# Kernel optimization log

Hardware: AMD Instinct MI355X
Metric: run time of the kernel (lower is better)

## Reference

```python
import jax, jax.numpy as jnp
import numpy as np

B, L, D, H, FFN = 4, 1024, 1024, 16, 4096
DPH = D // H
EPS = 1e-5

def layer_norm(x, g, b):
    mu = jnp.mean(x, axis=-1, keepdims=True)
    var = jnp.mean(jnp.square(x - mu), axis=-1, keepdims=True)
    return (x - mu) * jax.lax.rsqrt(var + EPS) * g + b

def setup_inputs() -> dict:
    key = jax.random.key(0)
    ks = jax.random.split(key, 12)
    s = 0.02
    return {
        "inputs": jax.random.normal(ks[0], (B, L, D), dtype=jnp.float32),
        "Wq": jax.random.normal(ks[1], (D, D), dtype=jnp.float32) * s,
        "bq": jnp.zeros((D,), jnp.float32),
        "Wk": jax.random.normal(ks[2], (D, D), dtype=jnp.float32) * s,
        "bk": jnp.zeros((D,), jnp.float32),
        "Wv": jax.random.normal(ks[3], (D, D), dtype=jnp.float32) * s,
        "bv": jnp.zeros((D,), jnp.float32),
        "Wo": jax.random.normal(ks[4], (D, D), dtype=jnp.float32) * s,
        "bo": jnp.zeros((D,), jnp.float32),
        "ln1_g": jnp.ones((D,), jnp.float32),
        "ln1_b": jnp.zeros((D,), jnp.float32),
        "W1": jax.random.normal(ks[5], (D, FFN), dtype=jnp.float32) * s,  # conv1d k=1 == linear
        "b1": jnp.zeros((FFN,), jnp.float32),
        "W2": jax.random.normal(ks[6], (FFN, D), dtype=jnp.float32) * s,
        "b2": jnp.zeros((D,), jnp.float32),
        "ln2_g": jnp.ones((D,), jnp.float32),
        "ln2_b": jnp.zeros((D,), jnp.float32),
    }

def reference(inputs, Wq, bq, Wk, bk, Wv, bv, Wo, bo, ln1_g, ln1_b,
              W1, b1, W2, b2, ln2_g, ln2_b):
    residual = inputs
    # QKV projections, then the original's raw view(B*H, L, DPH) split (NOT a transpose split)
    q = (inputs @ Wq + bq).reshape(B * H, L, DPH)
    k = (inputs @ Wk + bk).reshape(B * H, L, DPH)
    v = (inputs @ Wv + bv).reshape(B * H, L, DPH)
    scale = DPH ** -0.5
    scores = jnp.einsum('bqd,bkd->bqk', q, k) * scale  # [B*H, L, L]
    attention = jax.nn.softmax(scores, axis=-1)
    context = jnp.einsum('bqk,bkd->bqd', attention, v).reshape(B, L, D)
    out = context @ Wo + bo
    out = layer_norm(residual + out, ln1_g, ln1_b)
    # Positionwise FFN: two 1x1 conv1d == two linears with relu
    ffn = jax.nn.relu(out @ W1 + b1) @ W2 + b2
    out = layer_norm(out + ffn, ln2_g, ln2_b)
    return out, attention
```

## Files before the change

### kernel.cpp

```cpp
#include <hip/hip_runtime.h>
#include <hip/hip_bf16.h>
#include <stdint.h>


using bf16_t  = __hip_bfloat16;
using short8  = __attribute__((ext_vector_type(8))) short;
using short4v = __attribute__((ext_vector_type(4))) short;
using f32x4   = __attribute__((ext_vector_type(4))) float;

#define DEV static __device__ __forceinline__

DEV short bfbits(float f) {
  bf16_t h = __float2bfloat16(f);
  union { bf16_t h; short s; } u; u.h = h; return u.s;
}

DEV void gload_lds16(const bf16_t* g, bf16_t* lds) {
  __builtin_amdgcn_global_load_lds(
      (const __attribute__((address_space(1))) void*)g,
      (__attribute__((address_space(3))) void*)lds, 16, 0, 0);
}

__global__ __launch_bounds__(256) void k_f32_to_bf16(const float* __restrict__ in,
                                                     bf16_t* __restrict__ out) {
  size_t i = ((size_t)blockIdx.x * 256 + threadIdx.x) * 4;
  f32x4 x = *(const f32x4*)(in + i);
  short4v o;
  o[0] = bfbits(x[0]); o[1] = bfbits(x[1]); o[2] = bfbits(x[2]); o[3] = bfbits(x[3]);
  *(short4v*)((short*)out + i) = o;
}

__global__ __launch_bounds__(256) void k_transpose_f32_bf16(const float* __restrict__ in,
                                                            bf16_t* __restrict__ out,
                                                            int R, int C) {
  __shared__ float tile[32][33];
  int tx = threadIdx.x & 31, ty = threadIdx.x >> 5;
  int r0 = blockIdx.y * 32, c0 = blockIdx.x * 32;
  #pragma unroll
  for (int i = 0; i < 4; ++i)
    tile[ty + i * 8][tx] = in[(size_t)(r0 + ty + i * 8) * C + c0 + tx];
  __syncthreads();
  #pragma unroll
  for (int i = 0; i < 4; ++i)
    out[(size_t)(c0 + ty + i * 8) * R + r0 + tx] = __float2bfloat16(tile[tx][ty + i * 8]);
}

__global__ __launch_bounds__(256) void k_transpose4_f32_bf16(
    const float* __restrict__ w0, const float* __restrict__ w1,
    const float* __restrict__ w2, const float* __restrict__ w3,
    bf16_t* __restrict__ o0, bf16_t* __restrict__ o1,
    bf16_t* __restrict__ o2, bf16_t* __restrict__ o3) {
  __shared__ float tile[32][33];
  const int zz = blockIdx.z;
  const float* in = zz == 0 ? w0 : zz == 1 ? w1 : zz == 2 ? w2 : w3;
  bf16_t* out = zz == 0 ? o0 : zz == 1 ? o1 : zz == 2 ? o2 : o3;
  int tx = threadIdx.x & 31, ty = threadIdx.x >> 5;
  int r0 = blockIdx.y * 32, c0 = blockIdx.x * 32;
  #pragma unroll
  for (int i = 0; i < 4; ++i)
    tile[ty + i * 8][tx] = in[(size_t)(r0 + ty + i * 8) * 1024 + c0 + tx];
  __syncthreads();
  #pragma unroll
  for (int i = 0; i < 4; ++i)
    out[(size_t)(c0 + ty + i * 8) * 1024 + r0 + tx] = __float2bfloat16(tile[tx][ty + i * 8]);
}

__global__ __launch_bounds__(256) void k_transpose_bf16_b(const bf16_t* __restrict__ in,
                                                          bf16_t* __restrict__ out,
                                                          int R, int C, long sIn, long sOut) {
  __shared__ bf16_t tile[32][33];
  const bf16_t* inz = in + (size_t)blockIdx.z * sIn;
  bf16_t* outz = out + (size_t)blockIdx.z * sOut;
  int tx = threadIdx.x & 31, ty = threadIdx.x >> 5;
  int r0 = blockIdx.y * 32, c0 = blockIdx.x * 32;
  #pragma unroll
  for (int i = 0; i < 4; ++i)
    tile[ty + i * 8][tx] = inz[(size_t)(r0 + ty + i * 8) * C + c0 + tx];
  __syncthreads();
  #pragma unroll
  for (int i = 0; i < 4; ++i)
    outz[(size_t)(c0 + ty + i * 8) * R + r0 + tx] = tile[tx][ty + i * 8];
}

template<int BM, int BN, bool ALPHA, bool BIAS, bool RELU, bool RESID,
         bool OUTF, bool OUTB, bool QKV3>
__global__ __launch_bounds__(256)
void k_gemm_bt(const bf16_t* __restrict__ A, const bf16_t* __restrict__ Bt,
               float* __restrict__ Cf, bf16_t* __restrict__ Cb,
               const float* __restrict__ bias, const float* __restrict__ bias2,
               const float* __restrict__ bias3, const float* __restrict__ resid,
               int Kdim, int lda, int ldb, int ldc, float alpha) {
  constexpr int BK = 32;
  constexpr int WTM = BM / 2, WTN = BN / 2;
  constexpr int MI = WTM / 16, NI = WTN / 16;
  __shared__ __align__(16) bf16_t sA[BM * BK];
  __shared__ __align__(16) bf16_t sB[BN * BK];

  const int tid = threadIdx.x;
  const int lane = tid & 63;
  const int wv = tid >> 6;
  const int wm = wv & 1, wn = wv >> 1;

  const int gx = gridDim.x;
  const int total = gx * gridDim.y;
  const int lin = blockIdx.y * gx + blockIdx.x;
  const int swz = (lin & 7) * (total >> 3) + (lin >> 3);
  const size_t m0 = (size_t)(swz / gx) * BM;
  const size_t n0 = (size_t)(swz % gx) * BN;

  f32x4 acc[MI][NI] = {};

  const int rr = lane >> 2, cc = (lane & 3) * 8;
  const bf16_t* Arow = A + (m0 + rr) * (size_t)lda + cc;
  const bf16_t* Brow = Bt + (n0 + rr) * (size_t)ldb + cc;

  const int fm = wm * WTM + (lane & 15);
  const int fn = wn * WTN + (lane & 15);
  const int fk = (lane >> 4) * 8;

  for (int k0 = 0; k0 < Kdim; k0 += BK) {
    #pragma unroll
    for (int j = 0; j < BM / 64; ++j) {
      int c = j * 4 + wv;
      gload_lds16(Arow + (size_t)c * 16 * lda + k0, sA + c * 512);
    }
    #pragma unroll
    for (int j = 0; j < BN / 64; ++j) {
      int c = j * 4 + wv;
      gload_lds16(Brow + (size_t)c * 16 * ldb + k0, sB + c * 512);
    }
    __syncthreads();

    short8 av[MI], bvv[NI];
    #pragma unroll
    for (int mi = 0; mi < MI; ++mi) av[mi] = *(const short8*)(sA + (fm + mi * 16) * BK + fk);
    #pragma unroll
    for (int ni = 0; ni < NI; ++ni) bvv[ni] = *(const short8*)(sB + (fn + ni * 16) * BK + fk);
    #pragma unroll
    for (int mi = 0; mi < MI; ++mi)
      #pragma unroll
      for (int ni = 0; ni < NI; ++ni)
        acc[mi][ni] = __builtin_amdgcn_mfma_f32_16x16x32_bf16(av[mi], bvv[ni],
                                                              acc[mi][ni], 0, 0, 0);
    __syncthreads();
  }

  const int tz = QKV3 ? (int)(n0 >> 10) : 0;
  const float* bp = BIAS ? (QKV3 ? (tz == 0 ? bias : (tz == 1 ? bias2 : bias3))
                                 : bias) : nullptr;
  bf16_t* cb = QKV3 ? (Cb + (size_t)tz * 4194304) : Cb;
  const float qscale = (QKV3 && tz == 0) ? 0.125f : 1.0f;
  const int col0 = (int)n0 + wn * WTN + (lane & 15);
  const int row0 = (int)m0 + wm * WTM + ((lane >> 4) << 2);
  #pragma unroll
  for (int ni = 0; ni < NI; ++ni) {
    const int col = col0 + ni * 16;
    const int colw = QKV3 ? (col & 1023) : col;
    const float bval = BIAS ? bp[colw] : 0.0f;
    #pragma unroll
    for (int mi = 0; mi < MI; ++mi) {
      #pragma unroll
      for (int r = 0; r < 4; ++r) {
        int row = row0 + mi * 16 + r;
        float v = acc[mi][ni][r];
        if (ALPHA) v *= alpha;
        v += bval;
        if (QKV3) v *= qscale;
        size_t off = (size_t)row * ldc + colw;
        if (RESID) v += resid[off];
        if (RELU) v = fmaxf(v, 0.0f);
        if (OUTF) Cf[off] = v;
        if (OUTB) cb[off] = __float2bfloat16(v);
      }
    }
  }
}

__global__ __launch_bounds__(256) void k_flash_attn(const bf16_t* __restrict__ Qb,
                                                    const bf16_t* __restrict__ Kb,
                                                    const bf16_t* __restrict__ Vt,
                                                    float* __restrict__ attn,
                                                    bf16_t* __restrict__ ctx) {
  __shared__ __align__(16) bf16_t sK[2][64][64];
  __shared__ __align__(16) bf16_t sV[2][64][64];
  __shared__ __align__(16) bf16_t sP[128][64];

  const int tid = threadIdx.x;
  const int lane = tid & 63;
  const int wv = tid >> 6;

  const int lin = blockIdx.y * 8 + blockIdx.x;
  const int swz = (lin & 7) * 64 + (lin >> 3);
  const int z = swz >> 3;
  const int m0 = (swz & 7) * 128;

  const bf16_t* Qz = Qb + (size_t)z * 65536;
  const bf16_t* Kz = Kb + (size_t)z * 65536;
  const bf16_t* Vz = Vt + (size_t)z * 65536;
  float* az = attn + (size_t)z * 1048576;
  bf16_t* cz = ctx + (size_t)z * 65536;

  const int sr = tid >> 3, sc = (tid & 7) * 8;
  const int scx = sc ^ ((sr & 7) << 3);

  const int fr = lane & 15;
  const int fk = (lane >> 4) * 8;
  const int crow = (lane >> 4) << 2;
  const int rko = (fr & 7) << 3;

  short8 qf[2][2];
  #pragma unroll
  for (int mi = 0; mi < 2; ++mi)
    #pragma unroll
    for (int ks = 0; ks < 2; ++ks)
      qf[mi][ks] = *(const short8*)(Qz + (size_t)(m0 + wv * 32 + mi * 16 + fr) * 64 +
                                    ks * 32 + fk);

  float m_ln[2][4], s_ln[2][4];
  #pragma unroll
  for (int mi = 0; mi < 2; ++mi)
    #pragma unroll
    for (int r = 0; r < 4; ++r) { m_ln[mi][r] = -1e30f; s_ln[mi][r] = 0.0f; }

  short8 kreg[2], vreg[2];

  #pragma unroll
  for (int j = 0; j < 2; ++j)
    kreg[j] = *(const short8*)(Kz + (size_t)(j * 32 + sr) * 64 + sc);
  #pragma unroll
  for (int j = 0; j < 2; ++j)
    *(short8*)(&sK[0][j * 32 + sr][scx]) = kreg[j];
  #pragma unroll
  for (int j = 0; j < 2; ++j)
    kreg[j] = *(const short8*)(Kz + (size_t)(64 + j * 32 + sr) * 64 + sc);
  __syncthreads();

  for (int c = 0; c < 16; ++c) {
    const int cur = c & 1;
    if (c + 1 < 16) {
      #pragma unroll
      for (int j = 0; j < 2; ++j)
        *(short8*)(&sK[cur ^ 1][j * 32 + sr][scx]) = kreg[j];
    }
    if (c + 2 < 16) {
      #pragma unroll
      for (int j = 0; j < 2; ++j)
        kreg[j] = *(const short8*)(Kz + (size_t)((c + 2) * 64 + j * 32 + sr) * 64 + sc);
    }
    f32x4 acc[2][4] = {};
    __builtin_amdgcn_s_setprio(1);
    #pragma unroll
    for (int ks = 0; ks < 2; ++ks) {
      short8 bf[4];
      #pragma unroll
      for (int ni = 0; ni < 4; ++ni)
        bf[ni] = *(const short8*)(&sK[cur][ni * 16 + fr][(ks * 32 + fk) ^ rko]);
      #pragma unroll
      for (int mi = 0; mi < 2; ++mi)
        #pragma unroll
        for (int ni = 0; ni < 4; ++ni)
          acc[mi][ni] = __builtin_amdgcn_mfma_f32_16x16x32_bf16(qf[mi][ks], bf[ni],
                                                                acc[mi][ni], 0, 0, 0);
    }
    __builtin_amdgcn_s_setprio(0);
    #pragma unroll
    for (int mi = 0; mi < 2; ++mi)
      #pragma unroll
      for (int r = 0; r < 4; ++r) {
        float cm = fmaxf(fmaxf(acc[mi][0][r], acc[mi][1][r]),
                         fmaxf(acc[mi][2][r], acc[mi][3][r]));
        float mo = m_ln[mi][r];
        float mn = fmaxf(mo, cm);
        float se = 0.0f;
        #pragma unroll
        for (int ni = 0; ni < 4; ++ni) se += __expf(acc[mi][ni][r] - mn);
        s_ln[mi][r] = s_ln[mi][r] * __expf(mo - mn) + se;
        m_ln[mi][r] = mn;
      }
    __syncthreads();
  }

  float m_run[2][4], inv_s[2][4];
  #pragma unroll
  for (int mi = 0; mi < 2; ++mi)
    #pragma unroll
    for (int r = 0; r < 4; ++r) {
      float m = m_ln[mi][r], s = s_ln[mi][r];
      #pragma unroll
      for (int o = 1; o < 16; o <<= 1) {
        float m2 = __shfl_xor(m, o, 64);
        float s2 = __shfl_xor(s, o, 64);
        float mn = fmaxf(m, m2);
        s = s * __expf(m - mn) + s2 * __expf(m2 - mn);
        m = mn;
      }
      m_run[mi][r] = m;
      inv_s[mi][r] = 1.0f / s;
    }

  #pragma unroll
  for (int j = 0; j < 2; ++j) {
    kreg[j] = *(const short8*)(Kz + (size_t)(j * 32 + sr) * 64 + sc);
    vreg[j] = *(const short8*)(Vz + (size_t)(j * 32 + sr) * 1024 + sc);
  }
  #pragma unroll
  for (int j = 0; j < 2; ++j) {
    *(short8*)(&sK[0][j * 32 + sr][scx]) = kreg[j];
    *(short8*)(&sV[0][j * 32 + sr][scx]) = vreg[j];
  }
  #pragma unroll
  for (int j = 0; j < 2; ++j) {
    kreg[j] = *(const short8*)(Kz + (size_t)(64 + j * 32 + sr) * 64 + sc);
    vreg[j] = *(const short8*)(Vz + (size_t)(j * 32 + sr) * 1024 + 64 + sc);
  }
  __syncthreads();

  f32x4 cacc[2][4] = {};
  for (int c = 0; c < 16; ++c) {
    const int cur = c & 1;
    const int c0 = c * 64;
    if (c + 1 < 16) {
      #pragma unroll
      for (int j = 0; j < 2; ++j) {
        *(short8*)(&sK[cur ^ 1][j * 32 + sr][scx]) = kreg[j];
        *(short8*)(&sV[cur ^ 1][j * 32 + sr][scx]) = vreg[j];
      }
    }
    if (c + 2 < 16) {
      #pragma unroll
      for (int j = 0; j < 2; ++j) {
        kreg[j] = *(const short8*)(Kz + (size_t)((c + 2) * 64 + j * 32 + sr) * 64 + sc);
        vreg[j] = *(const short8*)(Vz + (size_t)(j * 32 + sr) * 1024 + (c + 2) * 64 + sc);
      }
    }
    f32x4 acc[2][4] = {};
    __builtin_amdgcn_s_setprio(1);
    #pragma unroll
    for (int ks = 0; ks < 2; ++ks) {
      short8 bf[4];
      #pragma unroll
      for (int ni = 0; ni < 4; ++ni)
        bf[ni] = *(const short8*)(&sK[cur][ni * 16 + fr][(ks * 32 + fk) ^ rko]);
      #pragma unroll
      for (int mi = 0; mi < 2; ++mi)
        #pragma unroll
        for (int ni = 0; ni < 4; ++ni)
          acc[mi][ni] = __builtin_amdgcn_mfma_f32_16x16x32_bf16(qf[mi][ks], bf[ni],
                                                                acc[mi][ni], 0, 0, 0);
    }
    __builtin_amdgcn_s_setprio(0);
    #pragma unroll
    for (int mi = 0; mi < 2; ++mi)
      #pragma unroll
      for (int ni = 0; ni < 4; ++ni)
        #pragma unroll
        for (int r = 0; r < 4; ++r) {
          int row = wv * 32 + mi * 16 + crow + r;
          float p = __expf(acc[mi][ni][r] - m_run[mi][r]) * inv_s[mi][r];
          __builtin_nontemporal_store(p, &az[(size_t)(m0 + row) * 1024 + c0 + ni * 16 + fr]);
          sP[row][(ni * 16 + fr) ^ (((crow + r) & 7) << 3)] = __float2bfloat16(p);
        }
    asm volatile("s_waitcnt lgkmcnt(0)" ::: "memory");
    __builtin_amdgcn_sched_barrier(0);
    __builtin_amdgcn_s_setprio(1);
    #pragma unroll
    for (int ks = 0; ks < 2; ++ks) {
      short8 pa[2], vb[4];
      #pragma unroll
      for (int mi = 0; mi < 2; ++mi)
        pa[mi] = *(const short8*)(&sP[wv * 32 + mi * 16 + fr][(ks * 32 + fk) ^ rko]);
      #pragma unroll
      for (int ni = 0; ni < 4; ++ni)
        vb[ni] = *(const short8*)(&sV[cur][ni * 16 + fr][(ks * 32 + fk) ^ rko]);
      #pragma unroll
      for (int mi = 0; mi < 2; ++mi)
        #pragma unroll
        for (int ni = 0; ni < 4; ++ni)
          cacc[mi][ni] = __builtin_amdgcn_mfma_f32_16x16x32_bf16(pa[mi], vb[ni],
                                                                 cacc[mi][ni], 0, 0, 0);
    }
    __builtin_amdgcn_s_setprio(0);
    __syncthreads();
  }

  #pragma unroll
  for (int mi = 0; mi < 2; ++mi)
    #pragma unroll
    for (int ni = 0; ni < 4; ++ni)
      #pragma unroll
      for (int r = 0; r < 4; ++r) {
        int row = wv * 32 + mi * 16 + crow + r;
        cz[(size_t)(m0 + row) * 64 + ni * 16 + fr] = __float2bfloat16(cacc[mi][ni][r]);
      }
}

__global__ __launch_bounds__(256) void k_layernorm(float* __restrict__ io,
                                                   bf16_t* __restrict__ ob,
                                                   const float* __restrict__ g,
                                                   const float* __restrict__ bta) {
  float* r = io + (size_t)blockIdx.x * 1024;
  const int t = threadIdx.x;
  f32x4 x = *(const f32x4*)(r + t * 4);
  float s = x[0] + x[1] + x[2] + x[3];
  float s2 = x[0] * x[0] + x[1] * x[1] + x[2] * x[2] + x[3] * x[3];
  #pragma unroll
  for (int o = 32; o > 0; o >>= 1) { s += __shfl_xor(s, o, 64); s2 += __shfl_xor(s2, o, 64); }
  __shared__ float as[4], as2[4];
  if ((t & 63) == 0) { as[t >> 6] = s; as2[t >> 6] = s2; }
  __syncthreads();
  s = as[0] + as[1] + as[2] + as[3];
  s2 = as2[0] + as2[1] + as2[2] + as2[3];
  float mu = s * (1.0f / 1024.0f);
  float var = s2 * (1.0f / 1024.0f) - mu * mu;
  float rs = rsqrtf(var + 1e-5f);
  f32x4 gg = *(const f32x4*)(g + t * 4);
  f32x4 bb = *(const f32x4*)(bta + t * 4);
  f32x4 y;
  #pragma unroll
  for (int i = 0; i < 4; ++i) y[i] = (x[i] - mu) * rs * gg[i] + bb[i];
  *(f32x4*)(r + t * 4) = y;
  if (ob) {
    short4v o4;
    o4[0] = bfbits(y[0]); o4[1] = bfbits(y[1]); o4[2] = bfbits(y[2]); o4[3] = bfbits(y[3]);
    *(short4v*)((short*)ob + (size_t)blockIdx.x * 1024 + t * 4) = o4;
  }
}

extern "C" void kernel_launch(void* const* d_in, const int* in_sizes, int n_in,
                              void* d_out, int out_size, void* d_ws, size_t ws_size,
                              hipStream_t stream) {
  (void)in_sizes; (void)n_in; (void)out_size;
  const float* inputs = (const float*)d_in[0];
  const float* Wq = (const float*)d_in[1];  const float* bq = (const float*)d_in[2];
  const float* Wk = (const float*)d_in[3];  const float* bk = (const float*)d_in[4];
  const float* Wv = (const float*)d_in[5];  const float* bv = (const float*)d_in[6];
  const float* Wo = (const float*)d_in[7];  const float* bo = (const float*)d_in[8];
  const float* ln1g = (const float*)d_in[9];  const float* ln1b = (const float*)d_in[10];
  const float* W1 = (const float*)d_in[11]; const float* b1 = (const float*)d_in[12];
  const float* W2 = (const float*)d_in[13]; const float* b2 = (const float*)d_in[14];
  const float* ln2g = (const float*)d_in[15]; const float* ln2b = (const float*)d_in[16];

  const size_t MB = 1ull << 20;
  if (ws_size < 96 * MB) return;

  char* ws = (char*)d_ws;
  bf16_t* WQT  = (bf16_t*)(ws + 0 * MB);
  bf16_t* WKT  = (bf16_t*)(ws + 2 * MB);
  bf16_t* WVT  = (bf16_t*)(ws + 4 * MB);
  bf16_t* WOT  = (bf16_t*)(ws + 6 * MB);
  bf16_t* W1T  = (bf16_t*)(ws + 8 * MB);
  bf16_t* W2T  = (bf16_t*)(ws + 16 * MB);
  bf16_t* XB   = (bf16_t*)(ws + 24 * MB);
  bf16_t* QB   = (bf16_t*)(ws + 32 * MB);
  bf16_t* KB   = (bf16_t*)(ws + 40 * MB);
  bf16_t* VB   = (bf16_t*)(ws + 48 * MB);
  bf16_t* VT   = (bf16_t*)(ws + 56 * MB);
  bf16_t* CTX  = (bf16_t*)(ws + 24 * MB);
  float*  OUT1F = (float*)(ws + 40 * MB);
  bf16_t* OUT1B = (bf16_t*)(ws + 32 * MB);
  bf16_t* HB   = (bf16_t*)(ws + 64 * MB);

  float* outF = (float*)d_out;
  float* attn = outF + 4194304;

  k_f32_to_bf16<<<4096, 256, 0, stream>>>(inputs, XB);
  k_transpose4_f32_bf16<<<dim3(32, 32, 4), 256, 0, stream>>>(Wq, Wk, Wv, Wo,
                                                             WQT, WKT, WVT, WOT);
  k_transpose_f32_bf16<<<dim3(128, 32), 256, 0, stream>>>(W1, W1T, 1024, 4096);
  k_transpose_f32_bf16<<<dim3(32, 128), 256, 0, stream>>>(W2, W2T, 4096, 1024);

  k_gemm_bt<128, 128, false, true, false, false, false, true, true>
      <<<dim3(24, 32), 256, 0, stream>>>(XB, WQT, nullptr, QB, bq, bk, bv, nullptr,
                                         1024, 1024, 1024, 1024, 1.0f);

  k_transpose_bf16_b<<<dim3(2, 32, 64), 256, 0, stream>>>(VB, VT, 1024, 64, 65536, 65536);

  k_flash_attn<<<dim3(8, 64), 256, 0, stream>>>(QB, KB, VT, attn, CTX);

  k_gemm_bt<128, 64, false, true, false, true, true, false, false>
      <<<dim3(16, 32), 256, 0, stream>>>(CTX, WOT, OUT1F, nullptr, bo, nullptr, nullptr,
                                         inputs, 1024, 1024, 1024, 1024, 1.0f);

  k_layernorm<<<4096, 256, 0, stream>>>(OUT1F, OUT1B, ln1g, ln1b);

  k_gemm_bt<128, 128, false, true, true, false, false, true, false>
      <<<dim3(32, 32), 256, 0, stream>>>(OUT1B, W1T, nullptr, HB, b1, nullptr, nullptr,
                                         nullptr, 1024, 1024, 1024, 4096, 1.0f);

  k_gemm_bt<128, 64, false, true, false, true, true, false, false>
      <<<dim3(16, 32), 256, 0, stream>>>(HB, W2T, outF, nullptr, b2, nullptr, nullptr,
                                         OUT1F, 4096, 4096, 4096, 1024, 1.0f);

  k_layernorm<<<4096, 256, 0, stream>>>(outF, nullptr, ln2g, ln2b);
}
```

Baseline: 645.2 us.

## Restructure flash attention into single-wave blocks loading K/V fragments directly

The attention kernel goes from 256-thread blocks that cover 128 query rows to 64-thread single-wave blocks that cover 32 rows, with 2048 blocks instead of 512. The shared-memory K/V staging, the barriers and the priority hints are removed. Each wave now loads its K and V MFMA fragments straight from global memory into registers, double-buffered across chunks. This removes LDS traffic and block-wide syncs and adds more blocks for occupancy, but every wave re-reads K/V from global/L2 with no reuse across waves, which raises cache traffic.

```diff
diff --git a/kernel.cpp b/kernel.cpp
--- a/kernel.cpp
+++ b/kernel.cpp
@@ -176,23 +176,19 @@
   }
 }
 
-__global__ __launch_bounds__(256) void k_flash_attn(const bf16_t* __restrict__ Qb,
-                                                    const bf16_t* __restrict__ Kb,
-                                                    const bf16_t* __restrict__ Vt,
-                                                    float* __restrict__ attn,
-                                                    bf16_t* __restrict__ ctx) {
-  __shared__ __align__(16) bf16_t sK[2][64][64];
-  __shared__ __align__(16) bf16_t sV[2][64][64];
-  __shared__ __align__(16) bf16_t sP[128][64];
-
-  const int tid = threadIdx.x;
-  const int lane = tid & 63;
-  const int wv = tid >> 6;
-
-  const int lin = blockIdx.y * 8 + blockIdx.x;
-  const int swz = (lin & 7) * 64 + (lin >> 3);
-  const int z = swz >> 3;
-  const int m0 = (swz & 7) * 128;
+__global__ __launch_bounds__(64) void k_flash_attn(const bf16_t* __restrict__ Qb,
+                                                   const bf16_t* __restrict__ Kb,
+                                                   const bf16_t* __restrict__ Vt,
+                                                   float* __restrict__ attn,
+                                                   bf16_t* __restrict__ ctx) {
+  __shared__ __align__(16) bf16_t sP[32][64];
+
+  const int lane = threadIdx.x;
+
+  const int lin = blockIdx.x;
+  const int swz = (lin & 7) * 256 + (lin >> 3);
+  const int z = swz >> 5;
+  const int m0 = (swz & 31) * 32;
 
   const bf16_t* Qz = Qb + (size_t)z * 65536;
   const bf16_t* Kz = Kb + (size_t)z * 65536;
@@ -200,9 +196,6 @@
   float* az = attn + (size_t)z * 1048576;
   bf16_t* cz = ctx + (size_t)z * 65536;
 
-  const int sr = tid >> 3, sc = (tid & 7) * 8;
-  const int scx = sc ^ ((sr & 7) << 3);
-
   const int fr = lane & 15;
   const int fk = (lane >> 4) * 8;
   const int crow = (lane >> 4) << 2;
@@ -213,8 +206,26 @@
   for (int mi = 0; mi < 2; ++mi)
     #pragma unroll
     for (int ks = 0; ks < 2; ++ks)
-      qf[mi][ks] = *(const short8*)(Qz + (size_t)(m0 + wv * 32 + mi * 16 + fr) * 64 +
-                                    ks * 32 + fk);
+      qf[mi][ks] = *(const short8*)(Qz + (size_t)(m0 + mi * 16 + fr) * 64 + ks * 32 + fk);
+
+  const bf16_t* kbase = Kz + (size_t)fr * 64 + fk;
+  auto loadK = [&](short8 (&kf)[4][2], int c) {
+    const bf16_t* b = kbase + (size_t)c * 4096;
+    #pragma unroll
+    for (int ni = 0; ni < 4; ++ni)
+      #pragma unroll
+      for (int ks = 0; ks < 2; ++ks)
+        kf[ni][ks] = *(const short8*)(b + ni * 1024 + ks * 32);
+  };
+  const bf16_t* vbase = Vz + (size_t)fr * 1024 + fk;
+  auto loadV = [&](short8 (&vf)[4][2], int c) {
+    const bf16_t* b = vbase + c * 64;
+    #pragma unroll
+    for (int ni = 0; ni < 4; ++ni)
+      #pragma unroll
+      for (int ks = 0; ks < 2; ++ks)
+        vf[ni][ks] = *(const short8*)(b + (size_t)ni * 16 * 1024 + ks * 32);
+  };
 
   float m_ln[2][4], s_ln[2][4];
   #pragma unroll
@@ -222,47 +233,16 @@
     #pragma unroll
     for (int r = 0; r < 4; ++r) { m_ln[mi][r] = -1e30f; s_ln[mi][r] = 0.0f; }
 
-  short8 kreg[2], vreg[2];
-
-  #pragma unroll
-  for (int j = 0; j < 2; ++j)
-    kreg[j] = *(const short8*)(Kz + (size_t)(j * 32 + sr) * 64 + sc);
-  #pragma unroll
-  for (int j = 0; j < 2; ++j)
-    *(short8*)(&sK[0][j * 32 + sr][scx]) = kreg[j];
-  #pragma unroll
-  for (int j = 0; j < 2; ++j)
-    kreg[j] = *(const short8*)(Kz + (size_t)(64 + j * 32 + sr) * 64 + sc);
-  __syncthreads();
-
-  for (int c = 0; c < 16; ++c) {
-    const int cur = c & 1;
-    if (c + 1 < 16) {
-      #pragma unroll
-      for (int j = 0; j < 2; ++j)
-        *(short8*)(&sK[cur ^ 1][j * 32 + sr][scx]) = kreg[j];
-    }
-    if (c + 2 < 16) {
-      #pragma unroll
-      for (int j = 0; j < 2; ++j)
-        kreg[j] = *(const short8*)(Kz + (size_t)((c + 2) * 64 + j * 32 + sr) * 64 + sc);
-    }
+  auto qk_stats = [&](short8 (&kf)[4][2]) {
     f32x4 acc[2][4] = {};
-    __builtin_amdgcn_s_setprio(1);
-    #pragma unroll
-    for (int ks = 0; ks < 2; ++ks) {
-      short8 bf[4];
-      #pragma unroll
-      for (int ni = 0; ni < 4; ++ni)
-        bf[ni] = *(const short8*)(&sK[cur][ni * 16 + fr][(ks * 32 + fk) ^ rko]);
+    #pragma unroll
+    for (int ks = 0; ks < 2; ++ks)
       #pragma unroll
       for (int mi = 0; mi < 2; ++mi)
         #pragma unroll
         for (int ni = 0; ni < 4; ++ni)
-          acc[mi][ni] = __builtin_amdgcn_mfma_f32_16x16x32_bf16(qf[mi][ks], bf[ni],
+          acc[mi][ni] = __builtin_amdgcn_mfma_f32_16x16x32_bf16(qf[mi][ks], kf[ni][ks],
                                                                 acc[mi][ni], 0, 0, 0);
-    }
-    __builtin_amdgcn_s_setprio(0);
     #pragma unroll
     for (int mi = 0; mi < 2; ++mi)
       #pragma unroll
@@ -277,7 +257,16 @@
         s_ln[mi][r] = s_ln[mi][r] * __expf(mo - mn) + se;
         m_ln[mi][r] = mn;
       }
-    __syncthreads();
+  };
+
+  short8 kfA[4][2], kfB[4][2];
+
+  loadK(kfA, 0);
+  for (int c = 0; c < 16; c += 2) {
+    loadK(kfB, c + 1);
+    qk_stats(kfA);
+    if (c + 2 < 16) loadK(kfA, c + 2);
+    qk_stats(kfB);
   }
 
   float m_run[2][4], inv_s[2][4];
@@ -298,89 +287,53 @@
       inv_s[mi][r] = 1.0f / s;
     }
 
-  #pragma unroll
-  for (int j = 0; j < 2; ++j) {
-    kreg[j] = *(const short8*)(Kz + (size_t)(j * 32 + sr) * 64 + sc);
-    vreg[j] = *(const short8*)(Vz + (size_t)(j * 32 + sr) * 1024 + sc);
-  }
-  #pragma unroll
-  for (int j = 0; j < 2; ++j) {
-    *(short8*)(&sK[0][j * 32 + sr][scx]) = kreg[j];
-    *(short8*)(&sV[0][j * 32 + sr][scx]) = vreg[j];
-  }
-  #pragma unroll
-  for (int j = 0; j < 2; ++j) {
-    kreg[j] = *(const short8*)(Kz + (size_t)(64 + j * 32 + sr) * 64 + sc);
-    vreg[j] = *(const short8*)(Vz + (size_t)(j * 32 + sr) * 1024 + 64 + sc);
-  }
-  __syncthreads();
-
   f32x4 cacc[2][4] = {};
-  for (int c = 0; c < 16; ++c) {
-    const int cur = c & 1;
-    const int c0 = c * 64;
-    if (c + 1 < 16) {
-      #pragma unroll
-      for (int j = 0; j < 2; ++j) {
-        *(short8*)(&sK[cur ^ 1][j * 32 + sr][scx]) = kreg[j];
-        *(short8*)(&sV[cur ^ 1][j * 32 + sr][scx]) = vreg[j];
-      }
-    }
-    if (c + 2 < 16) {
-      #pragma unroll
-      for (int j = 0; j < 2; ++j) {
-        kreg[j] = *(const short8*)(Kz + (size_t)((c + 2) * 64 + j * 32 + sr) * 64 + sc);
-        vreg[j] = *(const short8*)(Vz + (size_t)(j * 32 + sr) * 1024 + (c + 2) * 64 + sc);
-      }
-    }
+  auto emit_pv = [&](short8 (&kf)[4][2], int c) {
+    short8 vf[4][2];
+    loadV(vf, c);
     f32x4 acc[2][4] = {};
-    __builtin_amdgcn_s_setprio(1);
-    #pragma unroll
-    for (int ks = 0; ks < 2; ++ks) {
-      short8 bf[4];
-      #pragma unroll
-      for (int ni = 0; ni < 4; ++ni)
-        bf[ni] = *(const short8*)(&sK[cur][ni * 16 + fr][(ks * 32 + fk) ^ rko]);
+    #pragma unroll
+    for (int ks = 0; ks < 2; ++ks)
       #pragma unroll
       for (int mi = 0; mi < 2; ++mi)
         #pragma unroll
         for (int ni = 0; ni < 4; ++ni)
-          acc[mi][ni] = __builtin_amdgcn_mfma_f32_16x16x32_bf16(qf[mi][ks], bf[ni],
+          acc[mi][ni] = __builtin_amdgcn_mfma_f32_16x16x32_bf16(qf[mi][ks], kf[ni][ks],
                                                                 acc[mi][ni], 0, 0, 0);
-    }
-    __builtin_amdgcn_s_setprio(0);
     #pragma unroll
     for (int mi = 0; mi < 2; ++mi)
       #pragma unroll
       for (int ni = 0; ni < 4; ++ni)
         #pragma unroll
         for (int r = 0; r < 4; ++r) {
-          int row = wv * 32 + mi * 16 + crow + r;
+          int rw = mi * 16 + crow + r;
           float p = __expf(acc[mi][ni][r] - m_run[mi][r]) * inv_s[mi][r];
-          __builtin_nontemporal_store(p, &az[(size_t)(m0 + row) * 1024 + c0 + ni * 16 + fr]);
-          sP[row][(ni * 16 + fr) ^ (((crow + r) & 7) << 3)] = __float2bfloat16(p);
+          __builtin_nontemporal_store(p, &az[(size_t)(m0 + rw) * 1024 + c * 64 + ni * 16 + fr]);
+          sP[rw][(ni * 16 + fr) ^ (((crow + r) & 7) << 3)] = __float2bfloat16(p);
         }
     asm volatile("s_waitcnt lgkmcnt(0)" ::: "memory");
     __builtin_amdgcn_sched_barrier(0);
-    __builtin_amdgcn_s_setprio(1);
     #pragma unroll
     for (int ks = 0; ks < 2; ++ks) {
-      short8 pa[2], vb[4];
+      short8 pa[2];
       #pragma unroll
       for (int mi = 0; mi < 2; ++mi)
-        pa[mi] = *(const short8*)(&sP[wv * 32 + mi * 16 + fr][(ks * 32 + fk) ^ rko]);
-      #pragma unroll
-      for (int ni = 0; ni < 4; ++ni)
-        vb[ni] = *(const short8*)(&sV[cur][ni * 16 + fr][(ks * 32 + fk) ^ rko]);
+        pa[mi] = *(const short8*)(&sP[mi * 16 + fr][(ks * 32 + fk) ^ rko]);
       #pragma unroll
       for (int mi = 0; mi < 2; ++mi)
         #pragma unroll
         for (int ni = 0; ni < 4; ++ni)
-          cacc[mi][ni] = __builtin_amdgcn_mfma_f32_16x16x32_bf16(pa[mi], vb[ni],
+          cacc[mi][ni] = __builtin_amdgcn_mfma_f32_16x16x32_bf16(pa[mi], vf[ni][ks],
                                                                  cacc[mi][ni], 0, 0, 0);
     }
-    __builtin_amdgcn_s_setprio(0);
-    __syncthreads();
+  };
+
+  loadK(kfA, 0);
+  for (int c = 0; c < 16; c += 2) {
+    loadK(kfB, c + 1);
+    emit_pv(kfA, c);
+    if (c + 2 < 16) loadK(kfA, c + 2);
+    emit_pv(kfB, c + 1);
   }
 
   #pragma unroll
@@ -389,8 +342,8 @@
     for (int ni = 0; ni < 4; ++ni)
       #pragma unroll
       for (int r = 0; r < 4; ++r) {
-        int row = wv * 32 + mi * 16 + crow + r;
-        cz[(size_t)(m0 + row) * 64 + ni * 16 + fr] = __float2bfloat16(cacc[mi][ni][r]);
+        int rw = mi * 16 + crow + r;
+        cz[(size_t)(m0 + rw) * 64 + ni * 16 + fr] = __float2bfloat16(cacc[mi][ni][r]);
       }
 }
 
@@ -475,7 +428,7 @@
 
   k_transpose_bf16_b<<<dim3(2, 32, 64), 256, 0, stream>>>(VB, VT, 1024, 64, 65536, 65536);
 
-  k_flash_attn<<<dim3(8, 64), 256, 0, stream>>>(QB, KB, VT, attn, CTX);
+  k_flash_attn<<<2048, 64, 0, stream>>>(QB, KB, VT, attn, CTX);
 
   k_gemm_bt<128, 64, false, true, false, true, true, false, false>
       <<<dim3(16, 32), 256, 0, stream>>>(CTX, WOT, OUT1F, nullptr, bo, nullptr, nullptr,
```

Measured after the change: 659.3 us. 2.2% more time.
